# Kernel optimization log

Measured on AMD Instinct MI355X. Metric: run time of the kernel, lower is better.

## Reference

```python
import jax, jax.numpy as jnp
import numpy as np

B, T, TC, C, CC, H = 2, 2048, 512, 1024, 512, 16
D = C // H  # head dim = 64


def setup_inputs() -> dict:
    key = jax.random.key(0)
    ks = jax.random.split(key, 18)
    w = lambda k, i, o: (jax.random.normal(k, (i, o), jnp.float32) / np.sqrt(i).astype(np.float32))
    return {
        "x": jax.random.normal(ks[0], (B, T, C), jnp.float32),
        "cross_input": jax.random.normal(ks[1], (B, TC, CC), jnp.float32),
        "Wk": w(ks[2], C, C),  "bk": jnp.zeros((C,), jnp.float32),
        "Wq": w(ks[3], C, C),  "bq": jnp.zeros((C,), jnp.float32),
        "Wv": w(ks[4], C, C),  "bv": jnp.zeros((C,), jnp.float32),
        "Wck": w(ks[5], CC, C), "bck": jnp.zeros((C,), jnp.float32),
        "Wcq": w(ks[6], C, C),  "bcq": jnp.zeros((C,), jnp.float32),
        "Wcv": w(ks[7], CC, C), "bcv": jnp.zeros((C,), jnp.float32),
        "Wp": w(ks[8], C, C),   "bp": jnp.zeros((C,), jnp.float32),
    }


def _heads(t):
    # [B, L, C] -> [B, H, L, D]
    b, l, _ = t.shape
    return t.reshape(b, l, H, D).transpose(0, 2, 1, 3)


def reference(x, cross_input, Wk, bk, Wq, bq, Wv, bv, Wck, bck, Wcq, bcq, Wcv, bcv, Wp, bp):
    scale = np.float32(1.0 / np.sqrt(D))
    q = _heads(x @ Wq + bq)
    k = _heads(x @ Wk + bk)
    v = _heads(x @ Wv + bv)
    # causal self-attention with materialized scores (faithful to original)
    att = jnp.einsum("bhqd,bhkd->bhqk", q, k) * scale
    causal = jnp.tril(jnp.ones((T, T), bool))
    att = jnp.where(causal[None, None], att, -jnp.inf)
    y = jnp.einsum("bhqk,bhkd->bhqd", jax.nn.softmax(att, axis=-1), v)
    # cross-attention (no mask)
    qc = _heads(x @ Wcq + bcq)
    kc = _heads(cross_input @ Wck + bck)
    vc = _heads(cross_input @ Wcv + bcv)
    attc = jnp.einsum("bhqd,bhkd->bhqk", qc, kc) * scale
    y = y + jnp.einsum("bhqk,bhkd->bhqd", jax.nn.softmax(attc, axis=-1), vc)
    # merge heads + output projection (dropout prob = 0 -> identity)
    y = y.transpose(0, 2, 1, 3).reshape(x.shape[0], T, C)
    return y @ Wp + bp
```

## Files before the change

kernel.cpp:

```cpp
#include <hip/hip_runtime.h>
#include <hip/hip_bf16.h>
#include <type_traits>

typedef __bf16 bf16;
typedef __bf16 bf16x8 __attribute__((ext_vector_type(8)));
typedef float floatx4 __attribute__((ext_vector_type(4)));

#define QLD 72
#define KLD 136

__device__ __forceinline__ void glds16(const bf16* g, bf16* l) {
  __builtin_amdgcn_global_load_lds((const __attribute__((address_space(1))) void*)g,
                                   (__attribute__((address_space(3))) void*)l, 16, 0, 0);
}

__global__ __launch_bounds__(256) void tobf16_kernel(const float* __restrict__ in,
                                                     bf16* __restrict__ out, int n4) {
  int i = blockIdx.x * 256 + threadIdx.x;
  if (i < n4) {
    float4 f = ((const float4*)in)[i];
    bf16 t[4] = {(bf16)f.x, (bf16)f.y, (bf16)f.z, (bf16)f.w};
    *(uint2*)&out[(long)i * 4] = *(const uint2*)t;
  }
}

__global__ __launch_bounds__(256) void concat4_kernel(float* __restrict__ dst,
                                                      const float* __restrict__ a,
                                                      const float* __restrict__ b,
                                                      const float* __restrict__ c,
                                                      const float* __restrict__ d) {
  int i = blockIdx.x * 256 + threadIdx.x;
  const float* s[4] = {a, b, c, d};
  dst[i] = s[i >> 10][i & 1023];
}

__global__ __launch_bounds__(256) void wtrans_kernel(const float* __restrict__ in,
                                                     bf16* __restrict__ out,
                                                     int R, int C) {
  __shared__ bf16 t[32][33];
  int tx = threadIdx.x, ty = threadIdx.y;
  int c = blockIdx.x * 32 + tx;
#pragma unroll
  for (int i = 0; i < 4; i++) {
    int r = blockIdx.y * 32 + ty + i * 8;
    t[ty + i * 8][tx] = (bf16)in[(long)r * C + c];
  }
  __syncthreads();
  int oc = blockIdx.y * 32 + tx;
#pragma unroll
  for (int i = 0; i < 4; i++) {
    int orr = blockIdx.x * 32 + ty + i * 8;
    out[(long)orr * R + oc] = t[tx][ty + i * 8];
  }
}

template <typename OutT>
__global__ __launch_bounds__(256, 3) void gemm128(const bf16* __restrict__ A,
                                                  const bf16* __restrict__ Bt,
                                                  const float* __restrict__ bias,
                                                  OutT* __restrict__ C,
                                                  int M, int N, int K, int ldc,
                                                  bf16* __restrict__ Vt,
                                                  int vcol0, int vcol1, int Lt, int tok_shift) {
  __shared__ alignas(16) bf16 As[128 * 32];
  __shared__ alignas(16) bf16 Bs[128 * 32];
  const int tid = threadIdx.x, wave = tid >> 6, lane = tid & 63;
  const int l16 = lane & 15, l4 = lane >> 4;
  const int wm = wave & 1, wn = wave >> 1;
  const int n0 = blockIdx.x * 128, m0 = blockIdx.y * 128;
  const int lrow = lane >> 2, lch = (lane & 3) * 8;

  floatx4 acc[4][4];
#pragma unroll
  for (int mt = 0; mt < 4; mt++)
#pragma unroll
    for (int nt = 0; nt < 4; nt++) acc[mt][nt] = (floatx4){0.f, 0.f, 0.f, 0.f};

  const bf16* Ag = A + (long)(m0 + wave * 32 + lrow) * K + lch;
  const bf16* Bg = Bt + (long)(n0 + wave * 32 + lrow) * K + lch;
  bf16* Al = &As[(wave * 32) * 32];
  bf16* Bl = &Bs[(wave * 32) * 32];

  for (int k0 = 0; k0 < K; k0 += 32) {
    __syncthreads();
    glds16(Ag + k0, Al);
    glds16(Ag + k0 + (long)16 * K, Al + 16 * 32);
    glds16(Bg + k0, Bl);
    glds16(Bg + k0 + (long)16 * K, Bl + 16 * 32);
    __syncthreads();
    bf16x8 a[4], b[4];
#pragma unroll
    for (int mt = 0; mt < 4; mt++) a[mt] = *(const bf16x8*)&As[(wm * 64 + mt * 16 + l16) * 32 + l4 * 8];
#pragma unroll
    for (int nt = 0; nt < 4; nt++) b[nt] = *(const bf16x8*)&Bs[(wn * 64 + nt * 16 + l16) * 32 + l4 * 8];
#pragma unroll
    for (int mt = 0; mt < 4; mt++)
#pragma unroll
      for (int nt = 0; nt < 4; nt++)
        acc[mt][nt] = __builtin_amdgcn_mfma_f32_16x16x32_bf16(a[mt], b[nt], acc[mt][nt], 0, 0, 0);
  }

  const bool vpath = (vcol0 >= 0) && (n0 >= vcol0) && (n0 < vcol1);
  if (!vpath) {
    const int coladj = (vcol0 >= 0 && n0 >= vcol1) ? (vcol1 - vcol0) : 0;
#pragma unroll
    for (int nt = 0; nt < 4; nt++) {
      int col = n0 + wn * 64 + nt * 16 + l16;
      float bv = bias[col];
#pragma unroll
      for (int mt = 0; mt < 4; mt++)
#pragma unroll
        for (int r = 0; r < 4; r++) {
          int row = m0 + wm * 64 + mt * 16 + l4 * 4 + r;
          float v = acc[mt][nt][r] + bv;
          if constexpr (std::is_same_v<OutT, float>) C[(long)row * ldc + col - coladj] = v;
          else                                       C[(long)row * ldc + col - coladj] = (bf16)v;
        }
    }
  } else {
#pragma unroll
    for (int nt = 0; nt < 4; nt++) {
      int col = n0 + wn * 64 + nt * 16 + l16;
      int c = col - vcol0, hh = c >> 6, dd = c & 63;
      float bv = bias[col];
#pragma unroll
      for (int mt = 0; mt < 4; mt++) {
        int t0 = m0 + wm * 64 + mt * 16 + l4 * 4;
        int bb = t0 >> tok_shift, t = t0 & ((1 << tok_shift) - 1);
        bf16 tmp[4];
#pragma unroll
        for (int r = 0; r < 4; r++) tmp[r] = (bf16)(acc[mt][nt][r] + bv);
        *(uint2*)&Vt[(((long)bb * 16 + hh) * 64 + dd) * Lt + t] = *(const uint2*)tmp;
      }
    }
  }
}

__global__ __launch_bounds__(256, 2) void attn_kernel(const bf16* __restrict__ QKQc,
                                                      const bf16* __restrict__ VtB,
                                                      const bf16* __restrict__ KcB,
                                                      const bf16* __restrict__ VctB,
                                                      bf16* __restrict__ Y) {
  __shared__ alignas(16) bf16 Qs[64 * QLD];
  __shared__ alignas(16) bf16 Ks[128 * QLD];
  __shared__ alignas(16) bf16 Vts[64 * KLD];
  __shared__ alignas(16) bf16 Ps[64 * KLD];
  const int tid = threadIdx.x, wave = tid >> 6, lane = tid & 63;
  const int l16 = lane & 15, l4 = lane >> 4;
  const int h = blockIdx.y, b = blockIdx.z;

  float o_self[4][4];
  float m_i[4], l_i[4];
  floatx4 oacc[4];

  for (int jj = 0; jj < 2; jj++) {
    const int qt = jj ? (31 - (int)blockIdx.x) : (int)blockIdx.x;
    const int q0 = qt * 64;
    const int qrow0 = q0 + wave * 16 + l4 * 4;

    for (int phase = 0; phase < 2; phase++) {
      const bf16* Qb;
      const bf16* Kb;
      const bf16* Vtb;
      int kstr, vtstr, nkt;
      if (phase == 0) {
        Qb = QKQc + (long)b * 2048 * 3072 + h * 64;
        Kb = Qb + 1024;                      kstr = 3072;
        Vtb = VtB + ((long)b * 16 + h) * 64 * 2048;  vtstr = 2048;
        nkt = (qt + 2) >> 1;
      } else {
        Qb = QKQc + (long)b * 2048 * 3072 + h * 64 + 2048;
        Kb = KcB + (long)b * 512 * 1024 + h * 64;    kstr = 1024;
        Vtb = VctB + ((long)b * 16 + h) * 64 * 512;  vtstr = 512;
        nkt = 4;
      }

      __syncthreads();
#pragma unroll
      for (int i = 0; i < 2; i++) {
        int idx = tid + i * 256, row = idx >> 3, ch = (idx & 7) * 8;
        bf16x8 qv = *(const bf16x8*)(Qb + (long)(q0 + row) * 3072 + ch);
#pragma unroll
        for (int j = 0; j < 8; j++) qv[j] = (bf16)((float)qv[j] * 0.125f);
        *(bf16x8*)&Qs[row * QLD + ch] = qv;
      }
#pragma unroll
      for (int r = 0; r < 4; r++) { m_i[r] = -__builtin_inff(); l_i[r] = 0.f; }
#pragma unroll
      for (int nt = 0; nt < 4; nt++) oacc[nt] = (floatx4){0.f, 0.f, 0.f, 0.f};

      bf16x8 kreg[4], vreg[4];
#pragma unroll
      for (int c = 0; c < 4; c++) {
        int idx = tid + c * 256;
        kreg[c] = *(const bf16x8*)(Kb + (long)(idx >> 3) * kstr + (idx & 7) * 8);
        vreg[c] = *(const bf16x8*)(Vtb + (long)(idx >> 4) * vtstr + (idx & 15) * 8);
      }

      for (int kt = 0; kt < nkt; kt++) {
        const int k0 = kt * 128;
        __syncthreads();
#pragma unroll
        for (int c = 0; c < 4; c++) {
          int idx = tid + c * 256;
          *(bf16x8*)&Ks[(idx >> 3) * QLD + (idx & 7) * 8] = kreg[c];
          *(bf16x8*)&Vts[(idx >> 4) * KLD + (idx & 15) * 8] = vreg[c];
        }
        __syncthreads();
        if (kt + 1 < nkt) {
          const int kn = k0 + 128;
#pragma unroll
          for (int c = 0; c < 4; c++) {
            int idx = tid + c * 256;
            kreg[c] = *(const bf16x8*)(Kb + (long)(kn + (idx >> 3)) * kstr + (idx & 7) * 8);
            vreg[c] = *(const bf16x8*)(Vtb + (long)(idx >> 4) * vtstr + kn + (idx & 15) * 8);
          }
        }

        floatx4 sacc[8];
#pragma unroll
        for (int nt = 0; nt < 8; nt++) sacc[nt] = (floatx4){0.f, 0.f, 0.f, 0.f};
#pragma unroll
        for (int ds = 0; ds < 2; ds++) {
          bf16x8 af = *(const bf16x8*)&Qs[(wave * 16 + l16) * QLD + ds * 32 + l4 * 8];
#pragma unroll
          for (int nt = 0; nt < 8; nt++) {
            bf16x8 bfr = *(const bf16x8*)&Ks[(nt * 16 + l16) * QLD + ds * 32 + l4 * 8];
            sacc[nt] = __builtin_amdgcn_mfma_f32_16x16x32_bf16(af, bfr, sacc[nt], 0, 0, 0);
          }
        }
        if (phase == 0 && kt == nkt - 1) {
          int keyb = k0 + l16;
#pragma unroll
          for (int nt = 0; nt < 8; nt++) {
            int key = keyb + nt * 16;
#pragma unroll
            for (int r = 0; r < 4; r++)
              if (key > qrow0 + r) sacc[nt][r] = -__builtin_inff();
          }
        }
        float mx[4];
#pragma unroll
        for (int r = 0; r < 4; r++) mx[r] = m_i[r];
#pragma unroll
        for (int nt = 0; nt < 8; nt++)
#pragma unroll
          for (int r = 0; r < 4; r++) mx[r] = fmaxf(mx[r], sacc[nt][r]);
#pragma unroll
        for (int r = 0; r < 4; r++) {
#pragma unroll
          for (int off = 1; off < 16; off <<= 1) mx[r] = fmaxf(mx[r], __shfl_xor(mx[r], off));
        }
        float alpha[4], rs[4];
#pragma unroll
        for (int r = 0; r < 4; r++) {
          alpha[r] = __expf(m_i[r] - mx[r]);
          m_i[r] = mx[r];
          rs[r] = 0.f;
        }
#pragma unroll
        for (int nt = 0; nt < 8; nt++)
#pragma unroll
          for (int r = 0; r < 4; r++) {
            float p = __expf(sacc[nt][r] - mx[r]);
            rs[r] += p;
            Ps[(wave * 16 + l4 * 4 + r) * KLD + nt * 16 + l16] = (bf16)p;
          }
#pragma unroll
        for (int r = 0; r < 4; r++) {
#pragma unroll
          for (int off = 1; off < 16; off <<= 1) rs[r] += __shfl_xor(rs[r], off);
          l_i[r] = l_i[r] * alpha[r] + rs[r];
        }
#pragma unroll
        for (int nt = 0; nt < 4; nt++)
#pragma unroll
          for (int r = 0; r < 4; r++) oacc[nt][r] *= alpha[r];
#pragma unroll
        for (int ks = 0; ks < 4; ks++) {
          bf16x8 af = *(const bf16x8*)&Ps[(wave * 16 + l16) * KLD + ks * 32 + l4 * 8];
#pragma unroll
          for (int nt = 0; nt < 4; nt++) {
            bf16x8 bfr = *(const bf16x8*)&Vts[(nt * 16 + l16) * KLD + ks * 32 + l4 * 8];
            oacc[nt] = __builtin_amdgcn_mfma_f32_16x16x32_bf16(af, bfr, oacc[nt], 0, 0, 0);
          }
        }
      }

      if (phase == 0) {
#pragma unroll
        for (int r = 0; r < 4; r++) {
          float inv = 1.0f / l_i[r];
#pragma unroll
          for (int nt = 0; nt < 4; nt++) o_self[nt][r] = oacc[nt][r] * inv;
        }
      } else {
#pragma unroll
        for (int r = 0; r < 4; r++) {
          float inv = 1.0f / l_i[r];
          long row = (long)b * 2048 + q0 + wave * 16 + l4 * 4 + r;
#pragma unroll
          for (int nt = 0; nt < 4; nt++) {
            int col = h * 64 + nt * 16 + l16;
            Y[row * 1024 + col] = (bf16)(o_self[nt][r] + oacc[nt][r] * inv);
          }
        }
      }
    }
  }
}

extern "C" void kernel_launch(void* const* d_in, const int* in_sizes, int n_in,
                              void* d_out, int out_size, void* d_ws, size_t ws_size,
                              hipStream_t stream) {
  const float* x   = (const float*)d_in[0];
  const float* xc  = (const float*)d_in[1];
  const float* Wk  = (const float*)d_in[2];  const float* bk  = (const float*)d_in[3];
  const float* Wq  = (const float*)d_in[4];  const float* bq  = (const float*)d_in[5];
  const float* Wv  = (const float*)d_in[6];  const float* bv  = (const float*)d_in[7];
  const float* Wck = (const float*)d_in[8];  const float* bck = (const float*)d_in[9];
  const float* Wcq = (const float*)d_in[10]; const float* bcq = (const float*)d_in[11];
  const float* Wcv = (const float*)d_in[12]; const float* bcv = (const float*)d_in[13];
  const float* Wp  = (const float*)d_in[14]; const float* bp  = (const float*)d_in[15];

  char* ws = (char*)d_ws;
  const size_t MB = 1ull << 20;
  bf16*  WT_all = (bf16*)(ws + 0);
  bf16*  WC_all = (bf16*)(ws + 8 * MB);
  bf16*  WpT    = (bf16*)(ws + 10 * MB);
  bf16*  xbf    = (bf16*)(ws + 12 * MB);
  bf16*  Yb     = xbf;
  bf16*  xcbf   = (bf16*)(ws + 20 * MB);
  float* bias4  = (float*)(ws + 21 * MB);
  float* biasc  = (float*)(ws + 21 * MB + 65536);
  bf16*  QKQc   = (bf16*)(ws + 22 * MB);
  bf16*  VtB    = (bf16*)(ws + 46 * MB);
  bf16*  KcB    = (bf16*)(ws + 54 * MB);
  bf16*  VctB   = (bf16*)(ws + 56 * MB);

  tobf16_kernel<<<4096, 256, 0, stream>>>(x, xbf, 1048576);
  tobf16_kernel<<<512, 256, 0, stream>>>(xc, xcbf, 131072);

  dim3 tb(32, 8);
  wtrans_kernel<<<dim3(32, 32), tb, 0, stream>>>(Wq,  WT_all + 0ll * 1024 * 1024, 1024, 1024);
  wtrans_kernel<<<dim3(32, 32), tb, 0, stream>>>(Wk,  WT_all + 1ll * 1024 * 1024, 1024, 1024);
  wtrans_kernel<<<dim3(32, 32), tb, 0, stream>>>(Wv,  WT_all + 2ll * 1024 * 1024, 1024, 1024);
  wtrans_kernel<<<dim3(32, 32), tb, 0, stream>>>(Wcq, WT_all + 3ll * 1024 * 1024, 1024, 1024);
  wtrans_kernel<<<dim3(32, 16), tb, 0, stream>>>(Wck, WC_all + 0ll * 1024 * 512, 512, 1024);
  wtrans_kernel<<<dim3(32, 16), tb, 0, stream>>>(Wcv, WC_all + 1ll * 1024 * 512, 512, 1024);
  wtrans_kernel<<<dim3(32, 32), tb, 0, stream>>>(Wp,  WpT, 1024, 1024);

  concat4_kernel<<<16, 256, 0, stream>>>(bias4, bq, bk, bv, bcq);
  concat4_kernel<<<8, 256, 0, stream>>>(biasc, bck, bcv, bck, bcv);

  gemm128<bf16><<<dim3(32, 32), 256, 0, stream>>>(xbf, WT_all, bias4, QKQc,
                                                  4096, 4096, 1024, 3072,
                                                  VtB, 2048, 3072, 2048, 11);
  gemm128<bf16><<<dim3(16, 8), 256, 0, stream>>>(xcbf, WC_all, biasc, KcB,
                                                 1024, 2048, 512, 1024,
                                                 VctB, 1024, 2048, 512, 9);

  attn_kernel<<<dim3(16, 16, 2), 256, 0, stream>>>(QKQc, VtB, KcB, VctB, Yb);

  gemm128<float><<<dim3(8, 32), 256, 0, stream>>>(Yb, WpT, bp, (float*)d_out,
                                                  4096, 1024, 1024, 1024,
                                                  nullptr, -1, -1, 0, 0);
}
```

Measured before the change: 292.9 us.

## Fuse prep kernels, restructure attention with transposed scores and register-resident P

Merges the bf16 conversion, bias concat and seven weight-transpose launches into one prep kernel to cut launch overhead. The attention kernel now computes S^T (K as A operand), so each lane owns one query row and needs only two cross-lane shuffles for max and sum. P is passed to the PV MFMA through register shuffles instead of an LDS round trip, which drops the Ps buffer and allows 3 blocks per CU. It also switches to exp2 with log2e folded into the Q scale, and launches one q-tile per block (64 tiles ordered heaviest first) instead of pairing tiles for load balance.

```diff
diff --git a/kernel.cpp b/kernel.cpp
--- a/kernel.cpp
+++ b/kernel.cpp
@@ -9,48 +9,70 @@
 #define QLD 72
 #define KLD 136
 
+#if __has_builtin(__builtin_amdgcn_exp2f)
+#define EXP2(x) __builtin_amdgcn_exp2f(x)
+#else
+#define EXP2(x) exp2f(x)
+#endif
+
 __device__ __forceinline__ void glds16(const bf16* g, bf16* l) {
   __builtin_amdgcn_global_load_lds((const __attribute__((address_space(1))) void*)g,
                                    (__attribute__((address_space(3))) void*)l, 16, 0, 0);
 }
 
-__global__ __launch_bounds__(256) void tobf16_kernel(const float* __restrict__ in,
-                                                     bf16* __restrict__ out, int n4) {
-  int i = blockIdx.x * 256 + threadIdx.x;
-  if (i < n4) {
-    float4 f = ((const float4*)in)[i];
+__device__ __forceinline__ unsigned pack_bf16(float a, float b) {
+  unsigned short ua = __builtin_bit_cast(unsigned short, (bf16)a);
+  unsigned short ub = __builtin_bit_cast(unsigned short, (bf16)b);
+  return (unsigned)ua | ((unsigned)ub << 16);
+}
+
+struct PrepArgs {
+  const float* x; const float* xc;
+  bf16* xbf; bf16* xcbf;
+  const float* b4[4];
+  const float* bc[2];
+  float* bias4; float* biasc;
+  const float* W[7];
+  bf16* WT[7];
+};
+
+__global__ __launch_bounds__(256) void prep_kernel(PrepArgs a) {
+  __shared__ bf16 tsh[32][33];
+  const int bx = blockIdx.x, tid = threadIdx.x;
+  if (bx < 4096) {
+    int i = bx * 256 + tid;
+    float4 f = ((const float4*)a.x)[i];
     bf16 t[4] = {(bf16)f.x, (bf16)f.y, (bf16)f.z, (bf16)f.w};
-    *(uint2*)&out[(long)i * 4] = *(const uint2*)t;
-  }
-}
-
-__global__ __launch_bounds__(256) void concat4_kernel(float* __restrict__ dst,
-                                                      const float* __restrict__ a,
-                                                      const float* __restrict__ b,
-                                                      const float* __restrict__ c,
-                                                      const float* __restrict__ d) {
-  int i = blockIdx.x * 256 + threadIdx.x;
-  const float* s[4] = {a, b, c, d};
-  dst[i] = s[i >> 10][i & 1023];
-}
-
-__global__ __launch_bounds__(256) void wtrans_kernel(const float* __restrict__ in,
-                                                     bf16* __restrict__ out,
-                                                     int R, int C) {
-  __shared__ bf16 t[32][33];
-  int tx = threadIdx.x, ty = threadIdx.y;
-  int c = blockIdx.x * 32 + tx;
-#pragma unroll
-  for (int i = 0; i < 4; i++) {
-    int r = blockIdx.y * 32 + ty + i * 8;
-    t[ty + i * 8][tx] = (bf16)in[(long)r * C + c];
-  }
-  __syncthreads();
-  int oc = blockIdx.y * 32 + tx;
-#pragma unroll
-  for (int i = 0; i < 4; i++) {
-    int orr = blockIdx.x * 32 + ty + i * 8;
-    out[(long)orr * R + oc] = t[tx][ty + i * 8];
+    *(uint2*)&a.xbf[(long)i * 4] = *(const uint2*)t;
+  } else if (bx < 4608) {
+    int i = (bx - 4096) * 256 + tid;
+    float4 f = ((const float4*)a.xc)[i];
+    bf16 t[4] = {(bf16)f.x, (bf16)f.y, (bf16)f.z, (bf16)f.w};
+    *(uint2*)&a.xcbf[(long)i * 4] = *(const uint2*)t;
+  } else if (bx < 4632) {
+    int lb = bx - 4608;
+    if (lb < 16) { int i = lb * 256 + tid; a.bias4[i] = a.b4[i >> 10][i & 1023]; }
+    else         { int i = (lb - 16) * 256 + tid; a.biasc[i] = a.bc[i >> 10][i & 1023]; }
+  } else {
+    int t = bx - 4632, w, R, bxw, byw;
+    if (t < 5120) { w = t >> 10; R = 1024; int l = t & 1023; bxw = l & 31; byw = l >> 5; }
+    else { int t2 = t - 5120; w = 5 + (t2 >> 9); R = 512; int l = t2 & 511; bxw = l & 31; byw = l >> 5; }
+    const float* in = a.W[w];
+    bf16* out = a.WT[w];
+    int tx = tid & 31, ty = tid >> 5;
+    int c = bxw * 32 + tx;
+#pragma unroll
+    for (int i = 0; i < 4; i++) {
+      int r = byw * 32 + ty + i * 8;
+      tsh[ty + i * 8][tx] = (bf16)in[(long)r * 1024 + c];
+    }
+    __syncthreads();
+    int oc = byw * 32 + tx;
+#pragma unroll
+    for (int i = 0; i < 4; i++) {
+      int orr = bxw * 32 + ty + i * 8;
+      out[(long)orr * R + oc] = tsh[tx][ty + i * 8];
+    }
   }
 }
 
@@ -136,7 +158,7 @@
   }
 }
 
-__global__ __launch_bounds__(256, 2) void attn_kernel(const bf16* __restrict__ QKQc,
+__global__ __launch_bounds__(256, 3) void attn_kernel(const bf16* __restrict__ QKQc,
                                                       const bf16* __restrict__ VtB,
                                                       const bf16* __restrict__ KcB,
                                                       const bf16* __restrict__ VctB,
@@ -144,167 +166,157 @@
   __shared__ alignas(16) bf16 Qs[64 * QLD];
   __shared__ alignas(16) bf16 Ks[128 * QLD];
   __shared__ alignas(16) bf16 Vts[64 * KLD];
-  __shared__ alignas(16) bf16 Ps[64 * KLD];
   const int tid = threadIdx.x, wave = tid >> 6, lane = tid & 63;
   const int l16 = lane & 15, l4 = lane >> 4;
-  const int h = blockIdx.y, b = blockIdx.z;
-
-  float o_self[4][4];
-  float m_i[4], l_i[4];
+  const int qt = 31 - (int)blockIdx.x, h = blockIdx.y, b = blockIdx.z;
+  const int q0 = qt * 64;
+  const int qa = q0 + wave * 16 + l16;
+
+  float o_self[16];
+  float m_i, l_i;
   floatx4 oacc[4];
 
-  for (int jj = 0; jj < 2; jj++) {
-    const int qt = jj ? (31 - (int)blockIdx.x) : (int)blockIdx.x;
-    const int q0 = qt * 64;
-    const int qrow0 = q0 + wave * 16 + l4 * 4;
-
-    for (int phase = 0; phase < 2; phase++) {
-      const bf16* Qb;
-      const bf16* Kb;
-      const bf16* Vtb;
-      int kstr, vtstr, nkt;
-      if (phase == 0) {
-        Qb = QKQc + (long)b * 2048 * 3072 + h * 64;
-        Kb = Qb + 1024;                      kstr = 3072;
-        Vtb = VtB + ((long)b * 16 + h) * 64 * 2048;  vtstr = 2048;
-        nkt = (qt + 2) >> 1;
-      } else {
-        Qb = QKQc + (long)b * 2048 * 3072 + h * 64 + 2048;
-        Kb = KcB + (long)b * 512 * 1024 + h * 64;    kstr = 1024;
-        Vtb = VctB + ((long)b * 16 + h) * 64 * 512;  vtstr = 512;
-        nkt = 4;
-      }
-
+  for (int phase = 0; phase < 2; phase++) {
+    const bf16* Qb;
+    const bf16* Kb;
+    const bf16* Vtb;
+    int kstr, vtstr, nkt;
+    if (phase == 0) {
+      Qb = QKQc + (long)b * 2048 * 3072 + h * 64;
+      Kb = Qb + 1024;                              kstr = 3072;
+      Vtb = VtB + ((long)b * 16 + h) * 64 * 2048;  vtstr = 2048;
+      nkt = (qt + 2) >> 1;
+    } else {
+      Qb = QKQc + (long)b * 2048 * 3072 + h * 64 + 2048;
+      Kb = KcB + (long)b * 512 * 1024 + h * 64;    kstr = 1024;
+      Vtb = VctB + ((long)b * 16 + h) * 64 * 512;  vtstr = 512;
+      nkt = 4;
+    }
+
+    __syncthreads();
+#pragma unroll
+    for (int i = 0; i < 2; i++) {
+      int idx = tid + i * 256, row = idx >> 3, ch = (idx & 7) * 8;
+      bf16x8 qv = *(const bf16x8*)(Qb + (long)(q0 + row) * 3072 + ch);
+#pragma unroll
+      for (int j = 0; j < 8; j++) qv[j] = (bf16)((float)qv[j] * 0.18033688f);
+      *(bf16x8*)&Qs[row * QLD + ch] = qv;
+    }
+    m_i = -__builtin_inff(); l_i = 0.f;
+#pragma unroll
+    for (int mt = 0; mt < 4; mt++) oacc[mt] = (floatx4){0.f, 0.f, 0.f, 0.f};
+
+    bf16x8 kreg[4], vreg[4];
+#pragma unroll
+    for (int c = 0; c < 4; c++) {
+      int idx = tid + c * 256;
+      kreg[c] = *(const bf16x8*)(Kb + (long)(idx >> 3) * kstr + (idx & 7) * 8);
+      vreg[c] = *(const bf16x8*)(Vtb + (long)(idx >> 4) * vtstr + (idx & 15) * 8);
+    }
+
+    for (int kt = 0; kt < nkt; kt++) {
+      const int k0 = kt * 128;
       __syncthreads();
-#pragma unroll
-      for (int i = 0; i < 2; i++) {
-        int idx = tid + i * 256, row = idx >> 3, ch = (idx & 7) * 8;
-        bf16x8 qv = *(const bf16x8*)(Qb + (long)(q0 + row) * 3072 + ch);
-#pragma unroll
-        for (int j = 0; j < 8; j++) qv[j] = (bf16)((float)qv[j] * 0.125f);
-        *(bf16x8*)&Qs[row * QLD + ch] = qv;
-      }
-#pragma unroll
-      for (int r = 0; r < 4; r++) { m_i[r] = -__builtin_inff(); l_i[r] = 0.f; }
-#pragma unroll
-      for (int nt = 0; nt < 4; nt++) oacc[nt] = (floatx4){0.f, 0.f, 0.f, 0.f};
-
-      bf16x8 kreg[4], vreg[4];
 #pragma unroll
       for (int c = 0; c < 4; c++) {
         int idx = tid + c * 256;
-        kreg[c] = *(const bf16x8*)(Kb + (long)(idx >> 3) * kstr + (idx & 7) * 8);
-        vreg[c] = *(const bf16x8*)(Vtb + (long)(idx >> 4) * vtstr + (idx & 15) * 8);
-      }
-
-      for (int kt = 0; kt < nkt; kt++) {
-        const int k0 = kt * 128;
-        __syncthreads();
+        *(bf16x8*)&Ks[(idx >> 3) * QLD + (idx & 7) * 8] = kreg[c];
+        *(bf16x8*)&Vts[(idx >> 4) * KLD + (idx & 15) * 8] = vreg[c];
+      }
+      __syncthreads();
+      if (kt + 1 < nkt) {
+        const int kn = k0 + 128;
 #pragma unroll
         for (int c = 0; c < 4; c++) {
           int idx = tid + c * 256;
-          *(bf16x8*)&Ks[(idx >> 3) * QLD + (idx & 7) * 8] = kreg[c];
-          *(bf16x8*)&Vts[(idx >> 4) * KLD + (idx & 15) * 8] = vreg[c];
-        }
-        __syncthreads();
-        if (kt + 1 < nkt) {
-          const int kn = k0 + 128;
-#pragma unroll
-          for (int c = 0; c < 4; c++) {
-            int idx = tid + c * 256;
-            kreg[c] = *(const bf16x8*)(Kb + (long)(kn + (idx >> 3)) * kstr + (idx & 7) * 8);
-            vreg[c] = *(const bf16x8*)(Vtb + (long)(idx >> 4) * vtstr + kn + (idx & 15) * 8);
-          }
-        }
-
-        floatx4 sacc[8];
-#pragma unroll
-        for (int nt = 0; nt < 8; nt++) sacc[nt] = (floatx4){0.f, 0.f, 0.f, 0.f};
-#pragma unroll
-        for (int ds = 0; ds < 2; ds++) {
-          bf16x8 af = *(const bf16x8*)&Qs[(wave * 16 + l16) * QLD + ds * 32 + l4 * 8];
-#pragma unroll
-          for (int nt = 0; nt < 8; nt++) {
-            bf16x8 bfr = *(const bf16x8*)&Ks[(nt * 16 + l16) * QLD + ds * 32 + l4 * 8];
-            sacc[nt] = __builtin_amdgcn_mfma_f32_16x16x32_bf16(af, bfr, sacc[nt], 0, 0, 0);
-          }
-        }
-        if (phase == 0 && kt == nkt - 1) {
-          int keyb = k0 + l16;
-#pragma unroll
-          for (int nt = 0; nt < 8; nt++) {
-            int key = keyb + nt * 16;
-#pragma unroll
-            for (int r = 0; r < 4; r++)
-              if (key > qrow0 + r) sacc[nt][r] = -__builtin_inff();
-          }
-        }
-        float mx[4];
-#pragma unroll
-        for (int r = 0; r < 4; r++) mx[r] = m_i[r];
-#pragma unroll
-        for (int nt = 0; nt < 8; nt++)
-#pragma unroll
-          for (int r = 0; r < 4; r++) mx[r] = fmaxf(mx[r], sacc[nt][r]);
-#pragma unroll
-        for (int r = 0; r < 4; r++) {
-#pragma unroll
-          for (int off = 1; off < 16; off <<= 1) mx[r] = fmaxf(mx[r], __shfl_xor(mx[r], off));
-        }
-        float alpha[4], rs[4];
-#pragma unroll
-        for (int r = 0; r < 4; r++) {
-          alpha[r] = __expf(m_i[r] - mx[r]);
-          m_i[r] = mx[r];
-          rs[r] = 0.f;
-        }
-#pragma unroll
-        for (int nt = 0; nt < 8; nt++)
-#pragma unroll
-          for (int r = 0; r < 4; r++) {
-            float p = __expf(sacc[nt][r] - mx[r]);
-            rs[r] += p;
-            Ps[(wave * 16 + l4 * 4 + r) * KLD + nt * 16 + l16] = (bf16)p;
-          }
-#pragma unroll
-        for (int r = 0; r < 4; r++) {
-#pragma unroll
-          for (int off = 1; off < 16; off <<= 1) rs[r] += __shfl_xor(rs[r], off);
-          l_i[r] = l_i[r] * alpha[r] + rs[r];
-        }
-#pragma unroll
-        for (int nt = 0; nt < 4; nt++)
-#pragma unroll
-          for (int r = 0; r < 4; r++) oacc[nt][r] *= alpha[r];
-#pragma unroll
-        for (int ks = 0; ks < 4; ks++) {
-          bf16x8 af = *(const bf16x8*)&Ps[(wave * 16 + l16) * KLD + ks * 32 + l4 * 8];
-#pragma unroll
-          for (int nt = 0; nt < 4; nt++) {
-            bf16x8 bfr = *(const bf16x8*)&Vts[(nt * 16 + l16) * KLD + ks * 32 + l4 * 8];
-            oacc[nt] = __builtin_amdgcn_mfma_f32_16x16x32_bf16(af, bfr, oacc[nt], 0, 0, 0);
-          }
-        }
-      }
-
-      if (phase == 0) {
-#pragma unroll
-        for (int r = 0; r < 4; r++) {
-          float inv = 1.0f / l_i[r];
-#pragma unroll
-          for (int nt = 0; nt < 4; nt++) o_self[nt][r] = oacc[nt][r] * inv;
-        }
-      } else {
-#pragma unroll
-        for (int r = 0; r < 4; r++) {
-          float inv = 1.0f / l_i[r];
-          long row = (long)b * 2048 + q0 + wave * 16 + l4 * 4 + r;
-#pragma unroll
-          for (int nt = 0; nt < 4; nt++) {
-            int col = h * 64 + nt * 16 + l16;
-            Y[row * 1024 + col] = (bf16)(o_self[nt][r] + oacc[nt][r] * inv);
-          }
-        }
+          kreg[c] = *(const bf16x8*)(Kb + (long)(kn + (idx >> 3)) * kstr + (idx & 7) * 8);
+          vreg[c] = *(const bf16x8*)(Vtb + (long)(idx >> 4) * vtstr + kn + (idx & 15) * 8);
+        }
+      }
+
+      floatx4 sacc[8];
+#pragma unroll
+      for (int mt = 0; mt < 8; mt++) sacc[mt] = (floatx4){0.f, 0.f, 0.f, 0.f};
+#pragma unroll
+      for (int ds = 0; ds < 2; ds++) {
+        bf16x8 qf = *(const bf16x8*)&Qs[(wave * 16 + l16) * QLD + ds * 32 + l4 * 8];
+#pragma unroll
+        for (int mt = 0; mt < 8; mt++) {
+          bf16x8 kf = *(const bf16x8*)&Ks[(mt * 16 + l16) * QLD + ds * 32 + l4 * 8];
+          sacc[mt] = __builtin_amdgcn_mfma_f32_16x16x32_bf16(kf, qf, sacc[mt], 0, 0, 0);
+        }
+      }
+      if (phase == 0 && kt == nkt - 1) {
+#pragma unroll
+        for (int mt = 0; mt < 8; mt++) {
+          int keyb = k0 + mt * 16 + l4 * 4;
+#pragma unroll
+          for (int r = 0; r < 4; r++)
+            if (keyb + r > qa) sacc[mt][r] = -__builtin_inff();
+        }
+      }
+      float mx = m_i;
+#pragma unroll
+      for (int mt = 0; mt < 8; mt++)
+#pragma unroll
+        for (int r = 0; r < 4; r++) mx = fmaxf(mx, sacc[mt][r]);
+      mx = fmaxf(mx, __shfl_xor(mx, 16));
+      mx = fmaxf(mx, __shfl_xor(mx, 32));
+      float alpha = EXP2(m_i - mx);
+      m_i = mx;
+      float rs = 0.f;
+      unsigned P2[8][2];
+#pragma unroll
+      for (int mt = 0; mt < 8; mt++) {
+        float p0 = EXP2(sacc[mt][0] - mx), p1 = EXP2(sacc[mt][1] - mx);
+        float p2 = EXP2(sacc[mt][2] - mx), p3 = EXP2(sacc[mt][3] - mx);
+        rs += (p0 + p1) + (p2 + p3);
+        P2[mt][0] = pack_bf16(p0, p1);
+        P2[mt][1] = pack_bf16(p2, p3);
+      }
+      rs += __shfl_xor(rs, 16);
+      rs += __shfl_xor(rs, 32);
+      l_i = l_i * alpha + rs;
+#pragma unroll
+      for (int mt = 0; mt < 4; mt++)
+#pragma unroll
+        for (int r = 0; r < 4; r++) oacc[mt][r] *= alpha;
+
+      const int srcA = l16 | ((lane & 16) << 1);
+      const int srcB = srcA + 16;
+      const bool hi = (lane & 32) != 0;
+#pragma unroll
+      for (int s = 0; s < 4; s++) {
+        unsigned a0 = __shfl(P2[2 * s][0], srcA), b0 = __shfl(P2[2 * s + 1][0], srcA);
+        unsigned a1 = __shfl(P2[2 * s][1], srcA), b1 = __shfl(P2[2 * s + 1][1], srcA);
+        unsigned a2 = __shfl(P2[2 * s][0], srcB), b2 = __shfl(P2[2 * s + 1][0], srcB);
+        unsigned a3 = __shfl(P2[2 * s][1], srcB), b3 = __shfl(P2[2 * s + 1][1], srcB);
+        uint4 u;
+        u.x = hi ? b0 : a0; u.y = hi ? b1 : a1; u.z = hi ? b2 : a2; u.w = hi ? b3 : a3;
+        bf16x8 pf = __builtin_bit_cast(bf16x8, u);
+#pragma unroll
+        for (int mt = 0; mt < 4; mt++) {
+          bf16x8 vf = *(const bf16x8*)&Vts[(mt * 16 + l16) * KLD + s * 32 + l4 * 8];
+          oacc[mt] = __builtin_amdgcn_mfma_f32_16x16x32_bf16(vf, pf, oacc[mt], 0, 0, 0);
+        }
+      }
+    }
+
+    if (phase == 0) {
+      float inv = 1.0f / l_i;
+#pragma unroll
+      for (int mt = 0; mt < 4; mt++)
+#pragma unroll
+        for (int r = 0; r < 4; r++) o_self[mt * 4 + r] = oacc[mt][r] * inv;
+    } else {
+      float inv = 1.0f / l_i;
+      long row = (long)b * 2048 + qa;
+#pragma unroll
+      for (int mt = 0; mt < 4; mt++) {
+        bf16 tmp[4];
+#pragma unroll
+        for (int r = 0; r < 4; r++) tmp[r] = (bf16)(o_self[mt * 4 + r] + oacc[mt][r] * inv);
+        *(uint2*)&Y[row * 1024 + h * 64 + mt * 16 + l4 * 4] = *(const uint2*)tmp;
       }
     }
   }
@@ -338,20 +350,19 @@
   bf16*  KcB    = (bf16*)(ws + 54 * MB);
   bf16*  VctB   = (bf16*)(ws + 56 * MB);
 
-  tobf16_kernel<<<4096, 256, 0, stream>>>(x, xbf, 1048576);
-  tobf16_kernel<<<512, 256, 0, stream>>>(xc, xcbf, 131072);
-
-  dim3 tb(32, 8);
-  wtrans_kernel<<<dim3(32, 32), tb, 0, stream>>>(Wq,  WT_all + 0ll * 1024 * 1024, 1024, 1024);
-  wtrans_kernel<<<dim3(32, 32), tb, 0, stream>>>(Wk,  WT_all + 1ll * 1024 * 1024, 1024, 1024);
-  wtrans_kernel<<<dim3(32, 32), tb, 0, stream>>>(Wv,  WT_all + 2ll * 1024 * 1024, 1024, 1024);
-  wtrans_kernel<<<dim3(32, 32), tb, 0, stream>>>(Wcq, WT_all + 3ll * 1024 * 1024, 1024, 1024);
-  wtrans_kernel<<<dim3(32, 16), tb, 0, stream>>>(Wck, WC_all + 0ll * 1024 * 512, 512, 1024);
-  wtrans_kernel<<<dim3(32, 16), tb, 0, stream>>>(Wcv, WC_all + 1ll * 1024 * 512, 512, 1024);
-  wtrans_kernel<<<dim3(32, 32), tb, 0, stream>>>(Wp,  WpT, 1024, 1024);
-
-  concat4_kernel<<<16, 256, 0, stream>>>(bias4, bq, bk, bv, bcq);
-  concat4_kernel<<<8, 256, 0, stream>>>(biasc, bck, bcv, bck, bcv);
+  PrepArgs pa;
+  pa.x = x; pa.xc = xc; pa.xbf = xbf; pa.xcbf = xcbf;
+  pa.b4[0] = bq; pa.b4[1] = bk; pa.b4[2] = bv; pa.b4[3] = bcq;
+  pa.bc[0] = bck; pa.bc[1] = bcv;
+  pa.bias4 = bias4; pa.biasc = biasc;
+  pa.W[0] = Wq;  pa.WT[0] = WT_all + 0ll * 1024 * 1024;
+  pa.W[1] = Wk;  pa.WT[1] = WT_all + 1ll * 1024 * 1024;
+  pa.W[2] = Wv;  pa.WT[2] = WT_all + 2ll * 1024 * 1024;
+  pa.W[3] = Wcq; pa.WT[3] = WT_all + 3ll * 1024 * 1024;
+  pa.W[4] = Wp;  pa.WT[4] = WpT;
+  pa.W[5] = Wck; pa.WT[5] = WC_all + 0ll * 1024 * 512;
+  pa.W[6] = Wcv; pa.WT[6] = WC_all + 1ll * 1024 * 512;
+  prep_kernel<<<10776, 256, 0, stream>>>(pa);
 
   gemm128<bf16><<<dim3(32, 32), 256, 0, stream>>>(xbf, WT_all, bias4, QKQc,
                                                   4096, 4096, 1024, 3072,
@@ -360,7 +371,7 @@
                                                  1024, 2048, 512, 1024,
                                                  VctB, 1024, 2048, 512, 9);
 
-  attn_kernel<<<dim3(16, 16, 2), 256, 0, stream>>>(QKQc, VtB, KcB, VctB, Yb);
+  attn_kernel<<<dim3(32, 16, 2), 256, 0, stream>>>(QKQc, VtB, KcB, VctB, Yb);
 
   gemm128<float><<<dim3(8, 32), 256, 0, stream>>>(Yb, WpT, bp, (float*)d_out,
                                                   4096, 1024, 1024, 1024,
```

Result: slower. 302.6 us (+3.3%).
